# Kernel optimization log

Measured on AMD Instinct MI355X. Metric: run time of the kernel, lower is better.

Reference implementation:

```python
import jax, jax.numpy as jnp
import numpy as np

B, T, V, H, L = 32, 128, 50257, 1024, 2


def setup_inputs() -> dict:
    key = jax.random.key(0)
    ks = jax.random.split(key, 8)
    s_in = 0.02   # small init to keep gates unsaturated
    return {
        "tokens": jax.random.randint(ks[0], (B, T), 0, V, dtype=jnp.int32),
        "embedding": jax.random.normal(ks[1], (V, H), jnp.float32) * s_in,
        "W_ih": jax.random.normal(ks[2], (L, 4 * H, H), jnp.float32) * s_in,
        "W_hh": jax.random.normal(ks[3], (L, 4 * H, H), jnp.float32) * s_in,
        "b_ih": jax.random.normal(ks[4], (L, 4 * H), jnp.float32) * s_in,
        "b_hh": jax.random.normal(ks[5], (L, 4 * H), jnp.float32) * s_in,
        "W_out": jax.random.normal(ks[6], (V, H), jnp.float32) * s_in,
        "b_out": jax.random.normal(ks[7], (V,), jnp.float32) * s_in,
        "h0": jnp.zeros((L, B, H), jnp.float32),
        "c0": jnp.zeros((L, B, H), jnp.float32),
    }


def reference(tokens, embedding, W_ih, W_hh, b_ih, b_hh, W_out, b_out, h0, c0):
    # Teacher-forced LSTM LM: embed -> L-layer LSTM (PyTorch gate order i,f,g,o)
    # -> vocab projection -> log-softmax. Dropout is identity (p=0 / eval).
    x = embedding[tokens]                      # [B,T,H]
    xs = jnp.swapaxes(x, 0, 1)                 # [T,B,H] time-major for scan
    n_layers = W_ih.shape[0]

    def step(carry, x_t):
        h, c = carry                           # each [L,B,H]
        inp = x_t
        hs, cs = [], []
        for l in range(n_layers):
            gates = inp @ W_ih[l].T + b_ih[l] + h[l] @ W_hh[l].T + b_hh[l]  # [B,4H]
            i_g, f_g, g_g, o_g = jnp.split(gates, 4, axis=-1)
            i_g = jax.nn.sigmoid(i_g)
            f_g = jax.nn.sigmoid(f_g)
            g_g = jnp.tanh(g_g)
            o_g = jax.nn.sigmoid(o_g)
            c_new = f_g * c[l] + i_g * g_g
            h_new = o_g * jnp.tanh(c_new)
            hs.append(h_new)
            cs.append(c_new)
            inp = h_new
        return (jnp.stack(hs), jnp.stack(cs)), inp

    (hT, cT), outs = jax.lax.scan(step, (h0, c0), xs)   # outs: [T,B,H]
    outs = jnp.swapaxes(outs, 0, 1)                     # [B,T,H]
    logits = outs @ W_out.T + b_out                     # [B,T,V]
    logp = jax.nn.log_softmax(logits, axis=-1)
    return logp, hT, cT
```

## Files before the change

### kernel.cpp

```cpp
#include <hip/hip_runtime.h>
#include <cstdint>
#include <cstddef>

#define DEVI __device__ __forceinline__

typedef __attribute__((ext_vector_type(8))) short short8;
typedef __attribute__((ext_vector_type(4))) float f32x4;
using u16 = unsigned short;

constexpr int BSZ = 32, TSZ = 128, VSZ = 50257, HSZ = 1024;
constexpr int M4 = BSZ * TSZ;
constexpr int FH = 4 * HSZ;
constexpr long long OUT_LOGP = (long long)M4 * VSZ;
constexpr int NWRK = 192;
constexpr int LDSB = 147584;
constexpr int LDBF = 50258;

DEVI u16 f2bf(float f) {
  unsigned u = __float_as_uint(f);
  unsigned r = (u + 0x7fffu + ((u >> 16) & 1u)) >> 16;
  return (u16)r;
}
DEVI float bf2f(u16 u) { return __uint_as_float(((unsigned)u) << 16); }
DEVI float sigm(float x) { return 1.f / (1.f + __expf(-x)); }
DEVI float tanh_fast(float x) { return 1.f - 2.f / (1.f + __expf(2.f * x)); }

DEVI f32x4 mfma16(short8 a, short8 b, f32x4 c) {
  return __builtin_amdgcn_mfma_f32_16x16x32_bf16(a, b, c, 0, 0, 0);
}

DEVI void gld16(const void* g, void* l) {
  auto gp = (const __attribute__((address_space(1))) unsigned int*)g;
  auto lp = (__attribute__((address_space(3))) unsigned int*)l;
  __builtin_amdgcn_global_load_lds(gp, lp, 16, 0, 0);
}

DEVI void cohld16x16(const u16* base, short8 (&d)[16]) {
  asm volatile(
      "global_load_dwordx4 %0, %16, off sc0 sc1\n\t"
      "global_load_dwordx4 %1, %16, off offset:64 sc0 sc1\n\t"
      "global_load_dwordx4 %2, %16, off offset:128 sc0 sc1\n\t"
      "global_load_dwordx4 %3, %16, off offset:192 sc0 sc1\n\t"
      "global_load_dwordx4 %4, %16, off offset:256 sc0 sc1\n\t"
      "global_load_dwordx4 %5, %16, off offset:320 sc0 sc1\n\t"
      "global_load_dwordx4 %6, %16, off offset:384 sc0 sc1\n\t"
      "global_load_dwordx4 %7, %16, off offset:448 sc0 sc1\n\t"
      "global_load_dwordx4 %8, %16, off offset:512 sc0 sc1\n\t"
      "global_load_dwordx4 %9, %16, off offset:576 sc0 sc1\n\t"
      "global_load_dwordx4 %10, %16, off offset:640 sc0 sc1\n\t"
      "global_load_dwordx4 %11, %16, off offset:704 sc0 sc1\n\t"
      "global_load_dwordx4 %12, %16, off offset:768 sc0 sc1\n\t"
      "global_load_dwordx4 %13, %16, off offset:832 sc0 sc1\n\t"
      "global_load_dwordx4 %14, %16, off offset:896 sc0 sc1\n\t"
      "global_load_dwordx4 %15, %16, off offset:960 sc0 sc1\n\t"
      "s_waitcnt vmcnt(0)"
      : "=&v"(d[0]), "=&v"(d[1]), "=&v"(d[2]), "=&v"(d[3]),
        "=&v"(d[4]), "=&v"(d[5]), "=&v"(d[6]), "=&v"(d[7]),
        "=&v"(d[8]), "=&v"(d[9]), "=&v"(d[10]), "=&v"(d[11]),
        "=&v"(d[12]), "=&v"(d[13]), "=&v"(d[14]), "=&v"(d[15])
      : "v"(base)
      : "memory");
}
DEVI void cohst2_u16(u16* p0, u16 v0, u16* p1, u16 v1) {
  asm volatile(
      "global_store_short %0, %2, off sc0 sc1\n\t"
      "global_store_short %1, %3, off sc0 sc1\n\t"
      "s_waitcnt vmcnt(0)"
      :: "v"(p0), "v"(p1), "v"((unsigned)v0), "v"((unsigned)v1)
      : "memory");
}
DEVI void cohst1_u16(u16* p0, u16 v0) {
  asm volatile(
      "global_store_short %0, %1, off sc0 sc1\n\t"
      "s_waitcnt vmcnt(0)"
      :: "v"(p0), "v"((unsigned)v0)
      : "memory");
}
DEVI void flagst(unsigned* p, unsigned v) {
  __hip_atomic_store(p, v, __ATOMIC_RELAXED, __HIP_MEMORY_SCOPE_AGENT);
}
DEVI unsigned flagld(const unsigned* p) {
  return __hip_atomic_load(p, __ATOMIC_RELAXED, __HIP_MEMORY_SCOPE_AGENT);
}

DEVI void wait64(const unsigned* f, unsigned g, int l) {
  while (!__all((int)(flagld(f + l) >= g))) __builtin_amdgcn_s_sleep(1);
}
DEVI void wait128(const unsigned* f, unsigned g, int l) {
  for (;;) {
    unsigned a = flagld(f + l);
    unsigned b = flagld(f + 64 + l);
    if (__all((int)((a >= g) && (b >= g)))) break;
    __builtin_amdgcn_s_sleep(1);
  }
}

__global__ void prep_misc(const float* __restrict__ bih, const float* __restrict__ bhh,
                          float* __restrict__ bias0, float* __restrict__ rowsum,
                          unsigned* __restrict__ bar) {
  int i = blockIdx.x * 256 + threadIdx.x;
  if (i < FH) { bias0[i] = bih[i] + bhh[i]; rowsum[i] = 0.f; }
  if (i < 1024) bar[i] = 0u;
}

__global__ void prep_h(const float* __restrict__ h0, u16* __restrict__ H0,
                       u16* __restrict__ h1init) {
  int i = blockIdx.x * 256 + threadIdx.x;
  H0[i] = f2bf(h0[i]);
  h1init[i] = f2bf(h0[BSZ * HSZ + i]);
}

__global__ void cvt_bf16(const float* __restrict__ src, u16* __restrict__ dst, int n4) {
  int i = blockIdx.x * blockDim.x + threadIdx.x;
  int stride = gridDim.x * blockDim.x;
  for (; i < n4; i += stride) {
    float4 v = ((const float4*)src)[i];
    ushort4 o; o.x = f2bf(v.x); o.y = f2bf(v.y); o.z = f2bf(v.z); o.w = f2bf(v.w);
    ((ushort4*)dst)[i] = o;
  }
}

__global__ __launch_bounds__(256) void embed_kernel(const int* __restrict__ tok,
                                                    const float* __restrict__ emb,
                                                    u16* __restrict__ X) {
  int m = blockIdx.x;
  int t = m >> 5, b = m & 31;
  int token = tok[b * TSZ + t];
  const float4* src = (const float4*)(emb + (size_t)token * HSZ);
  int i = threadIdx.x;
  float4 v = src[i];
  ushort4 o; o.x = f2bf(v.x); o.y = f2bf(v.y); o.z = f2bf(v.z); o.w = f2bf(v.w);
  *(ushort4*)(X + (size_t)m * HSZ + i * 4) = o;
}

template <int EPI, bool BCVT, int MAP>
__global__ __launch_bounds__(256) void gemm_bt(const u16* __restrict__ A,
                                               const void* __restrict__ Bsrc,
                                               void* __restrict__ Cout,
                                               const float* __restrict__ bias,
                                               float* __restrict__ rowsum,
                                               int nm, int nn, int N, int K, int ldc) {
  __shared__ char smemg[16384];
  u16* As = (u16*)smemg;
  u16* Bs = (u16*)(smemg + 8192);
  float* epi = (float*)smemg;
  const int tid = threadIdx.x;
  int gsz = nm * nn;
  int id = blockIdx.x;
  int bm, bn;
  if constexpr (MAP == 1) {
    const int xcd = id & 7, idx = id >> 3;
    bn = idx >> 2;
    bm = (xcd << 2) + (idx & 3);
  } else {
    int wg = ((gsz & 7) == 0) ? (id % 8) * (gsz >> 3) + (id >> 3) : id;
    bm = wg % nm; bn = wg / nm;
  }
  const int m0 = bm * 128, n0 = bn * 128;
  const int l = tid & 63, wid = tid >> 6;
  const int wm = wid >> 1, wn = wid & 1;

  const int srow = tid >> 2, sq = tid & 3;
  const int arow0 = m0 + srow, arow1 = m0 + 64 + srow;
  int brow0 = n0 + srow;      if (brow0 > N - 1) brow0 = N - 1;
  int brow1 = n0 + 64 + srow; if (brow1 > N - 1) brow1 = N - 1;

  const u16* Bbf = (const u16*)Bsrc;
  const float* Bf32 = (const float*)Bsrc;
  u16* AsW = As + (size_t)(tid >> 6) * 512;
  u16* BsW = Bs + (size_t)(tid >> 6) * 512;

  f32x4 acc[4][4];
  f32x4 z = {0.f, 0.f, 0.f, 0.f};
#pragma unroll
  for (int a = 0; a < 4; ++a)
#pragma unroll
    for (int b = 0; b < 4; ++b) acc[a][b] = z;

  for (int k0 = 0; k0 < K; k0 += 32) {
    gld16(A + (size_t)arow0 * K + k0 + sq * 8, AsW);
    gld16(A + (size_t)arow1 * K + k0 + sq * 8, AsW + 2048);
    if (!BCVT) {
      gld16(Bbf + (size_t)brow0 * K + k0 + sq * 8, BsW);
      gld16(Bbf + (size_t)brow1 * K + k0 + sq * 8, BsW + 2048);
    } else {
      const float* s0 = Bf32 + (size_t)brow0 * K + k0 + sq * 8;
      const float* s1 = Bf32 + (size_t)brow1 * K + k0 + sq * 8;
      float4 x0 = *(const float4*)s0, y0 = *(const float4*)(s0 + 4);
      float4 x1 = *(const float4*)s1, y1 = *(const float4*)(s1 + 4);
      short8 v0, v1;
      v0[0]=(short)f2bf(x0.x); v0[1]=(short)f2bf(x0.y); v0[2]=(short)f2bf(x0.z); v0[3]=(short)f2bf(x0.w);
      v0[4]=(short)f2bf(y0.x); v0[5]=(short)f2bf(y0.y); v0[6]=(short)f2bf(y0.z); v0[7]=(short)f2bf(y0.w);
      v1[0]=(short)f2bf(x1.x); v1[1]=(short)f2bf(x1.y); v1[2]=(short)f2bf(x1.z); v1[3]=(short)f2bf(x1.w);
      v1[4]=(short)f2bf(y1.x); v1[5]=(short)f2bf(y1.y); v1[6]=(short)f2bf(y1.z); v1[7]=(short)f2bf(y1.w);
      *(short8*)&Bs[(size_t)tid * 8] = v0;
      *(short8*)&Bs[(size_t)tid * 8 + 2048] = v1;
    }
    __syncthreads();
    short8 af[4], bfr[4];
#pragma unroll
    for (int x = 0; x < 4; ++x) {
      int ar = wm * 64 + x * 16 + (l & 15);
      af[x] = *(const short8*)&As[ar * 32 + ((l >> 4) << 3)];
      int br = wn * 64 + x * 16 + (l & 15);
      bfr[x] = *(const short8*)&Bs[br * 32 + ((l >> 4) << 3)];
    }
#pragma unroll
    for (int mf = 0; mf < 4; ++mf)
#pragma unroll
      for (int nf = 0; nf < 4; ++nf)
        acc[mf][nf] = mfma16(af[mf], bfr[nf], acc[mf][nf]);
    __syncthreads();
  }

  if constexpr (EPI == 2) {
    u16* C = (u16*)Cout;
#pragma unroll
    for (int mf = 0; mf < 4; ++mf) {
      int rbase = m0 + wm * 64 + mf * 16 + ((l >> 4) << 2);
      float bvr[4];
#pragma unroll
      for (int j = 0; j < 4; ++j) bvr[j] = bias[rbase + j];
#pragma unroll
      for (int nf = 0; nf < 4; ++nf) {
        int cg = n0 + wn * 64 + nf * 16 + (l & 15);
#pragma unroll
        for (int j = 0; j < 4; ++j)
          C[(size_t)(rbase + j) * ldc + cg] = f2bf(acc[mf][nf][j] + bvr[j]);
      }
    }
  } else if constexpr (EPI == 3) {
    u16* C = (u16*)Cout;
    float* ep = epi + wid * 1024;
    const int lq4 = l >> 4, l15e = l & 15;
    float bv[4];
#pragma unroll
    for (int nf = 0; nf < 4; ++nf) {
      int cg = n0 + wn * 64 + nf * 16 + l15e;
      bv[nf] = (cg < N) ? bias[cg] : 0.f;
    }
    const int r8 = l >> 3, c8 = l & 7;
    const int colb8 = n0 + wn * 64 + c8 * 8;
#pragma unroll
    for (int mf = 0; mf < 4; ++mf) {
#pragma unroll
      for (int nf = 0; nf < 4; ++nf)
#pragma unroll
        for (int j = 0; j < 4; ++j)
          ep[(lq4 * 4 + j) * 64 + nf * 16 + l15e] = acc[mf][nf][j] + bv[nf];
      asm volatile("s_waitcnt lgkmcnt(0)" ::: "memory");
      __builtin_amdgcn_sched_barrier(0);
#pragma unroll
      for (int pass = 0; pass < 2; ++pass) {
        const int rr = pass * 8 + r8;
        f32x4 v0 = *(const f32x4*)&ep[rr * 64 + c8 * 8];
        f32x4 v1 = *(const f32x4*)&ep[rr * 64 + c8 * 8 + 4];
        const int row = m0 + wm * 64 + mf * 16 + rr;
        float e = 0.f;
        if (colb8 + 7 < N) {
          short8 o;
          o[0]=(short)f2bf(v0[0]); o[1]=(short)f2bf(v0[1]);
          o[2]=(short)f2bf(v0[2]); o[3]=(short)f2bf(v0[3]);
          o[4]=(short)f2bf(v1[0]); o[5]=(short)f2bf(v1[1]);
          o[6]=(short)f2bf(v1[2]); o[7]=(short)f2bf(v1[3]);
          *(short8*)&C[(size_t)row * ldc + colb8] = o;
          e = __expf(v0[0]) + __expf(v0[1]) + __expf(v0[2]) + __expf(v0[3]) +
              __expf(v1[0]) + __expf(v1[1]) + __expf(v1[2]) + __expf(v1[3]);
        } else {
#pragma unroll
          for (int kk = 0; kk < 8; ++kk) {
            float fv = (kk < 4) ? v0[kk] : v1[kk - 4];
            if (colb8 + kk < N) {
              C[(size_t)row * ldc + colb8 + kk] = f2bf(fv);
              e += __expf(fv);
            }
          }
        }
        e += __shfl_xor(e, 1, 8); e += __shfl_xor(e, 2, 8); e += __shfl_xor(e, 4, 8);
        if (c8 == 0) atomicAdd(&rowsum[row], e);
      }
      asm volatile("s_waitcnt lgkmcnt(0)" ::: "memory");
      __builtin_amdgcn_sched_barrier(0);
    }
  } else {
    float* C = (float*)Cout;
    float* ep = epi + wid * 1024;
    const int lq4 = l >> 4, l15e = l & 15;
    float bv[4];
#pragma unroll
    for (int nf = 0; nf < 4; ++nf) {
      int cg = n0 + wn * 64 + nf * 16 + l15e;
      bv[nf] = (cg < N) ? bias[cg] : 0.f;
    }
    const int colbase = n0 + wn * 64 + l15e * 4;
#pragma unroll
    for (int mf = 0; mf < 4; ++mf) {
#pragma unroll
      for (int nf = 0; nf < 4; ++nf)
#pragma unroll
        for (int j = 0; j < 4; ++j)
          ep[(lq4 * 4 + j) * 64 + nf * 16 + l15e] = acc[mf][nf][j] + bv[nf];
      asm volatile("s_waitcnt lgkmcnt(0)" ::: "memory");
      __builtin_amdgcn_sched_barrier(0);
#pragma unroll
      for (int pass = 0; pass < 4; ++pass) {
        const int rr = pass * 4 + lq4;
        f32x4 v = *(const f32x4*)&ep[rr * 64 + l15e * 4];
        const int row = m0 + wm * 64 + mf * 16 + rr;
        float e = 0.f;
        if (colbase + 3 < N) {
          *(f32x4*)&C[(size_t)row * ldc + colbase] = v;
          e = __expf(v[0]) + __expf(v[1]) + __expf(v[2]) + __expf(v[3]);
        } else {
#pragma unroll
          for (int kk = 0; kk < 4; ++kk)
            if (colbase + kk < N) {
              C[(size_t)row * ldc + colbase + kk] = v[kk];
              e += __expf(v[kk]);
            }
        }
        e += __shfl_xor(e, 1, 16); e += __shfl_xor(e, 2, 16);
        e += __shfl_xor(e, 4, 16); e += __shfl_xor(e, 8, 16);
        if (l15e == 0) atomicAdd(&rowsum[row], e);
      }
      asm volatile("s_waitcnt lgkmcnt(0)" ::: "memory");
      __builtin_amdgcn_sched_barrier(0);
    }
  }
}

struct LstmArgs {
  const u16* G0T;
  const float* Wih;
  const float* Whh;
  const float* bih, *bhh, *c0;
  u16* H0;
  u16* H1;
  const u16* h1init;
  float* out_hc;
  unsigned* bar;
};

DEVI void stage_row_q(const float* src, char* row, int sw, int q) {
  for (int kk = 0; kk < 256; kk += 8) {
    float4 x = *(const float4*)(src + kk);
    float4 y = *(const float4*)(src + kk + 4);
    short8 v;
    v[0]=(short)f2bf(x.x); v[1]=(short)f2bf(x.y); v[2]=(short)f2bf(x.z); v[3]=(short)f2bf(x.w);
    v[4]=(short)f2bf(y.x); v[5]=(short)f2bf(y.y); v[6]=(short)f2bf(y.z); v[7]=(short)f2bf(y.w);
    const int kbyte = (q * 256 + kk) * 2;
    *(short8*)(row + (kbyte ^ sw)) = v;
  }
}

DEVI short8 ldsB(const char* lds, int r, int kbyte) {
  return *(const short8*)(lds + (size_t)r * 2048 + (kbyte ^ ((r & 7) << 4)));
}

DEVI void part_wr(float* part, int wstride_log2, int wv, int R, int lq, f32x4 v) {
  *(f32x4*)&part[(wv << wstride_log2) + (R << 4) + ((lq ^ (R & 3)) << 2)] = v;
}
DEVI float part_rd(const float* part, int wstride_log2, int wv, int R, int c) {
  return part[(wv << wstride_log2) + (R << 4) + ((((c >> 2) ^ (R & 3)) << 2)) + (c & 3)];
}

__global__ __launch_bounds__(256, 1) void lstm_coop(LstmArgs A) {
  extern __shared__ char smem[];
  const int wg = blockIdx.x, tid = threadIdx.x;
  const int wv = tid >> 6, l = tid & 63;
  const int l15 = l & 15, lq = l >> 4;
  const int bh = wv >> 1, kh = wv & 1;

  if (wg < 64) {
    char* WL = smem;
    float* part = (float*)(smem + 131072);
    const int j0 = wg << 4;
    {
      const int R = tid >> 2, q = tid & 3;
      const int grow = ((R >> 4) << 10) + j0 + (R & 15);
      stage_row_q(A.Whh + (size_t)grow * HSZ + q * 256, WL + (size_t)R * 2048,
                  (R & 7) << 4, q);
    }
    const int uu = tid & 15, bb = tid >> 4;
    float cst[2];
    cst[0] = A.c0[(size_t)bb * HSZ + j0 + uu];
    cst[1] = A.c0[(size_t)(bb + 16) * HSZ + j0 + uu];
    __syncthreads();
    unsigned* myflag = A.bar + wg;

    for (int t = 0; t < TSZ; ++t) {
      float g0v[4][2];
      {
        const int col = t * 32;
#pragma unroll
        for (int g4 = 0; g4 < 4; ++g4) {
          const u16* gp = A.G0T + (size_t)((g4 << 10) + j0 + uu) * M4 + col;
          g0v[g4][0] = bf2f(gp[bb]);
          g0v[g4][1] = bf2f(gp[bb + 16]);
        }
      }
      if (t > 0) wait64(A.bar, (unsigned)t, l);
      const u16* hprev = A.H0 + (size_t)t * (BSZ * HSZ);
      const u16* hb = hprev + (size_t)(bh * 16 + l15) * HSZ + (kh << 9) + (lq << 3);
      short8 a[16];
      cohld16x16(hb, a);
      __builtin_amdgcn_sched_barrier(0);
      f32x4 acc[4];
      { f32x4 z = {0.f,0.f,0.f,0.f}; acc[0]=z; acc[1]=z; acc[2]=z; acc[3]=z; }
#pragma unroll
      for (int k = 0; k < 16; ++k) {
        const int kbyte = (((kh << 4) + k) << 6) + (lq << 4);
#pragma unroll
        for (int tr = 0; tr < 4; ++tr)
          acc[tr] = mfma16(a[k], ldsB(WL, (tr << 4) + l15, kbyte), acc[tr]);
      }
#pragma unroll
      for (int tr = 0; tr < 4; ++tr)
        part_wr(part, 10, wv, (tr << 4) + l15, lq, acc[tr]);
      __syncthreads();
      const bool last = (t == TSZ - 1);
      u16* hnext = A.H0 + (size_t)(t + 1) * (BSZ * HSZ);
      u16 hv[2];
#pragma unroll
      for (int pp = 0; pp < 2; ++pp) {
        const int b = bb + (pp << 4);
        float gi = g0v[0][pp], gf = g0v[1][pp], gg = g0v[2][pp], go = g0v[3][pp];
#pragma unroll
        for (int kh2 = 0; kh2 < 2; ++kh2) {
          const int w2 = (pp << 1) | kh2;
          gi += part_rd(part, 10, w2, uu, bb);
          gf += part_rd(part, 10, w2, 16 + uu, bb);
          gg += part_rd(part, 10, w2, 32 + uu, bb);
          go += part_rd(part, 10, w2, 48 + uu, bb);
        }
        float i_ = sigm(gi), f_ = sigm(gf), g_ = tanh_fast(gg), o_ = sigm(go);
        float c_ = f_ * cst[pp] + i_ * g_;
        cst[pp] = c_;
        float h_ = o_ * tanh_fast(c_);
        hv[pp] = f2bf(h_);
        if (last) {
          A.out_hc[(size_t)b * HSZ + j0 + uu] = h_;
          A.out_hc[2 * BSZ * HSZ + (size_t)b * HSZ + j0 + uu] = c_;
        }
      }
      cohst2_u16(hnext + (size_t)bb * HSZ + j0 + uu, hv[0],
                 hnext + (size_t)(bb + 16) * HSZ + j0 + uu, hv[1]);
      __syncthreads();
      if (tid == 0) flagst(myflag, (unsigned)(t + 1));
    }
  } else {
    char* WxL = smem;
    char* WhL = smem + 65536;
    float* part = (float*)(smem + 131072);
    float* biasL = (float*)(smem + 139264);
    const int lw = wg - 64;
    const int j1 = lw << 3;
    {
      const int rr = tid >> 2, q = tid & 3;
      const int r = rr & 31;
      const int grow = FH + ((r >> 3) << 10) + j1 + (r & 7);
      const float* base = (rr >= 32) ? A.Whh : A.Wih;
      char* dst = ((rr >= 32) ? WhL : WxL) + (size_t)r * 2048;
      stage_row_q(base + (size_t)grow * HSZ + q * 256, dst, (r & 7) << 4, q);
    }
    if (tid < 32) {
      const int grow = FH + ((tid >> 3) << 10) + j1 + (tid & 7);
      biasL[tid] = A.bih[grow] + A.bhh[grow];
    }
    const int uu = tid & 7, b1 = tid >> 3;
    float cst = A.c0[BSZ * HSZ + (size_t)b1 * HSZ + j1 + uu];
    __syncthreads();
    unsigned* myflag = A.bar + 64 + lw;

    for (int t = 0; t < TSZ; ++t) {
      wait64(A.bar, (unsigned)(t + 1), l);
      const u16* x1 = A.H0 + (size_t)(t + 1) * (BSZ * HSZ);
      const u16* xb = x1 + (size_t)(bh * 16 + l15) * HSZ + (kh << 9) + (lq << 3);
      short8 ax[16];
      cohld16x16(xb, ax);
      __builtin_amdgcn_sched_barrier(0);
      f32x4 acc[2];
      { f32x4 z = {0.f,0.f,0.f,0.f}; acc[0]=z; acc[1]=z; }
#pragma unroll
      for (int k = 0; k < 16; ++k) {
        const int kbyte = (((kh << 4) + k) << 6) + (lq << 4);
        acc[0] = mfma16(ax[k], ldsB(WxL, l15, kbyte), acc[0]);
        acc[1] = mfma16(ax[k], ldsB(WxL, 16 + l15, kbyte), acc[1]);
      }
      if (t > 0) wait128(A.bar + 64, (unsigned)t, l);
      const u16* hp = (t == 0) ? A.h1init : A.H1 + (size_t)(t - 1) * HSZ;
      const size_t hstr = (t == 0) ? (size_t)HSZ : (size_t)TSZ * HSZ;
      const u16* hbp = hp + (size_t)(bh * 16 + l15) * hstr + (kh << 9) + (lq << 3);
      short8 ah[16];
      cohld16x16(hbp, ah);
      __builtin_amdgcn_sched_barrier(0);
#pragma unroll
      for (int k = 0; k < 16; ++k) {
        const int kbyte = (((kh << 4) + k) << 6) + (lq << 4);
        acc[0] = mfma16(ah[k], ldsB(WhL, l15, kbyte), acc[0]);
        acc[1] = mfma16(ah[k], ldsB(WhL, 16 + l15, kbyte), acc[1]);
      }
#pragma unroll
      for (int tr = 0; tr < 2; ++tr)
        part_wr(part, 9, wv, (tr << 4) + l15, lq, acc[tr]);
      __syncthreads();
      const bool last = (t == TSZ - 1);
      {
        const int c = b1 & 15, ph = b1 >> 4;
        float gi = biasL[uu], gf = biasL[8 + uu], gg = biasL[16 + uu], go = biasL[24 + uu];
#pragma unroll
        for (int kh2 = 0; kh2 < 2; ++kh2) {
          const int w2 = (ph << 1) | kh2;
          gi += part_rd(part, 9, w2, uu, c);
          gf += part_rd(part, 9, w2, 8 + uu, c);
          gg += part_rd(part, 9, w2, 16 + uu, c);
          go += part_rd(part, 9, w2, 24 + uu, c);
        }
        float i_ = sigm(gi), f_ = sigm(gf), g_ = tanh_fast(gg), o_ = sigm(go);
        float c_ = f_ * cst + i_ * g_;
        cst = c_;
        float h_ = o_ * tanh_fast(c_);
        cohst1_u16(A.H1 + (size_t)b1 * (TSZ * HSZ) + (size_t)t * HSZ + j1 + uu, f2bf(h_));
        if (last) {
          A.out_hc[BSZ * HSZ + (size_t)b1 * HSZ + j1 + uu] = h_;
          A.out_hc[3 * BSZ * HSZ + (size_t)b1 * HSZ + j1 + uu] = c_;
        }
      }
      __syncthreads();
      if (tid == 0) flagst(myflag, (unsigned)(t + 1));
    }
  }
}

__global__ void lse_kernel(float* __restrict__ rowsum, int n) {
  int i = blockIdx.x * 256 + threadIdx.x;
  if (i < n) rowsum[i] = logf(rowsum[i]);
}

__global__ __launch_bounds__(256) void lsm_finish(float* __restrict__ C,
                                                  const float* __restrict__ lse, int Vd) {
  int row = blockIdx.y;
  size_t start = (size_t)row * (size_t)Vd;
  float s = lse[row];
  int i = blockIdx.x * 256 + threadIdx.x;
  int col = i * 4;
  if (col + 3 < Vd) {
    f32x4* p = (f32x4*)(C + start + col);
    f32x4 v = *p;
    v[0] -= s; v[1] -= s; v[2] -= s; v[3] -= s;
    *p = v;
  } else {
    for (int j = col; j < Vd; ++j) C[start + j] -= s;
  }
}

__global__ __launch_bounds__(256) void lsm_finish_bf(const u16* __restrict__ L,
                                                     float* __restrict__ out,
                                                     const float* __restrict__ lse,
                                                     int Vd, int ldl) {
  int row = blockIdx.y;
  float s = lse[row];
  int col = blockIdx.x * 2048 + threadIdx.x * 8;
  const u16* lp = L + (size_t)row * ldl;
  float* op = out + (size_t)row * Vd;
  if (col + 7 < Vd) {
    short8 v = *(const short8*)(lp + col);
    f32x4 a, b;
    a[0] = bf2f((u16)v[0]) - s; a[1] = bf2f((u16)v[1]) - s;
    a[2] = bf2f((u16)v[2]) - s; a[3] = bf2f((u16)v[3]) - s;
    b[0] = bf2f((u16)v[4]) - s; b[1] = bf2f((u16)v[5]) - s;
    b[2] = bf2f((u16)v[6]) - s; b[3] = bf2f((u16)v[7]) - s;
    *(f32x4*)(op + col) = a;
    *(f32x4*)(op + col + 4) = b;
  } else {
    for (int j = col; j < Vd; ++j) op[j] = bf2f(lp[j]) - s;
  }
}

extern "C" void kernel_launch(void* const* d_in, const int* in_sizes, int n_in,
                              void* d_out, int out_size, void* d_ws, size_t ws_size,
                              hipStream_t stream) {
  const int* tokens = (const int*)d_in[0];
  const float* emb = (const float*)d_in[1];
  const float* Wih = (const float*)d_in[2];
  const float* Whh = (const float*)d_in[3];
  const float* bih = (const float*)d_in[4];
  const float* bhh = (const float*)d_in[5];
  const float* Wout = (const float*)d_in[6];
  const float* bout = (const float*)d_in[7];
  const float* h0 = (const float*)d_in[8];
  const float* c0 = (const float*)d_in[9];
  float* out = (float*)d_out;

  char* w = (char*)d_ws;
  size_t o = 0;
  u16* Xbf = (u16*)(w + o);    o += (size_t)M4 * HSZ * 2;
  u16* Wih0bf = (u16*)(w + o); o += (size_t)FH * HSZ * 2;
  u16* G0T = (u16*)(w + o);    o += (size_t)FH * M4 * 2;
  u16* H0 = (u16*)(w + o);     o += (size_t)(TSZ + 1) * BSZ * HSZ * 2;
  u16* H1 = (u16*)(w + o);     o += (size_t)BSZ * TSZ * HSZ * 2;
  u16* h1init = (u16*)(w + o); o += (size_t)BSZ * HSZ * 2;
  float* bias0 = (float*)(w + o);  o += FH * 4;
  float* rowsum = (float*)(w + o); o += M4 * 4;
  unsigned* bar = (unsigned*)(w + o); o += 4096;
  u16* Woutbf = (u16*)(w + o);
  size_t need_full = o + (size_t)VSZ * HSZ * 2;
  u16* Lbf = (u16*)(w + need_full);
  size_t need_lbf = need_full + (size_t)M4 * LDBF * 2;
  const bool bcvt = (ws_size < need_full);
  const bool bf16c = (ws_size >= need_lbf);

  prep_misc<<<16, 256, 0, stream>>>(bih, bhh, bias0, rowsum, bar);
  prep_h<<<128, 256, 0, stream>>>(h0, H0, h1init);
  cvt_bf16<<<2048, 256, 0, stream>>>(Wih, Wih0bf, FH * HSZ / 4);
  if (!bcvt)
    cvt_bf16<<<4096, 256, 0, stream>>>(Wout, Woutbf, (int)((size_t)VSZ * HSZ / 4));
  embed_kernel<<<M4, 256, 0, stream>>>(tokens, emb, Xbf);
  gemm_bt<2, false, 0><<<32 * 32, 256, 0, stream>>>(Wih0bf, Xbf, G0T, bias0, nullptr,
                                                    32, 32, M4, HSZ, M4);

  LstmArgs la{G0T, Wih, Whh, bih, bhh, c0, H0, H1, h1init,
              out + (size_t)OUT_LOGP, bar};
  void* kargs[] = {&la};
  hipFuncSetAttribute((const void*)lstm_coop, hipFuncAttributeMaxDynamicSharedMemorySize, LDSB);
  hipLaunchCooperativeKernel((const void*)lstm_coop, dim3(NWRK), dim3(256), kargs, LDSB, stream);

  const int nn = (VSZ + 127) / 128;
  if (bf16c) {
    gemm_bt<3, false, 1><<<32 * nn, 256, 0, stream>>>(H1, Woutbf, Lbf, bout, rowsum,
                                                      32, nn, VSZ, HSZ, LDBF);
  } else if (!bcvt) {
    gemm_bt<1, false, 1><<<32 * nn, 256, 0, stream>>>(H1, Woutbf, out, bout, rowsum,
                                                      32, nn, VSZ, HSZ, VSZ);
  } else {
    gemm_bt<1, true, 1><<<32 * nn, 256, 0, stream>>>(H1, Wout, out, bout, rowsum,
                                                     32, nn, VSZ, HSZ, VSZ);
  }

  lse_kernel<<<16, 256, 0, stream>>>(rowsum, M4);
  if (bf16c)
    lsm_finish_bf<<<dim3(25, M4), 256, 0, stream>>>(Lbf, out, rowsum, VSZ, LDBF);
  else
    lsm_finish<<<dim3((VSZ + 1023) / 1024, M4), 256, 0, stream>>>(out, rowsum, VSZ);
}
```

Baseline: 1.807 ms.

## Overlap Wout bf16 conversion with LSTM recurrence using spare cooperative blocks

```diff
diff --git a/kernel.cpp b/kernel.cpp
--- a/kernel.cpp
+++ b/kernel.cpp
@@ -13,6 +13,7 @@
 constexpr int FH = 4 * HSZ;
 constexpr long long OUT_LOGP = (long long)M4 * VSZ;
 constexpr int NWRK = 192;
+constexpr int NBLK = 256;
 constexpr int LDSB = 147584;
 constexpr int LDBF = 50258;
 
@@ -339,6 +340,9 @@
   const u16* h1init;
   float* out_hc;
   unsigned* bar;
+  const float* Wout;
+  u16* Woutbf;
+  int docvt;
 };
 
 DEVI void stage_row_q(const float* src, char* row, int sw, int q) {
@@ -448,7 +452,7 @@
       __syncthreads();
       if (tid == 0) flagst(myflag, (unsigned)(t + 1));
     }
-  } else {
+  } else if (wg < NWRK) {
     char* WxL = smem;
     char* WhL = smem + 65536;
     float* part = (float*)(smem + 131072);
@@ -529,6 +533,19 @@
       __syncthreads();
       if (tid == 0) flagst(myflag, (unsigned)(t + 1));
     }
+  } else {
+    if (A.docvt) {
+      const int n4 = (int)((size_t)VSZ * HSZ / 4);
+      int i = (wg - NWRK) * 256 + tid;
+      const int stride = 64 * 256;
+      const float4* src = (const float4*)A.Wout;
+      ushort4* dst = (ushort4*)A.Woutbf;
+      for (; i < n4; i += stride) {
+        float4 v = src[i];
+        ushort4 o; o.x = f2bf(v.x); o.y = f2bf(v.y); o.z = f2bf(v.z); o.w = f2bf(v.w);
+        dst[i] = o;
+      }
+    }
   }
 }
 
@@ -556,10 +573,10 @@
 
 __global__ __launch_bounds__(256) void lsm_finish_bf(const u16* __restrict__ L,
                                                      float* __restrict__ out,
-                                                     const float* __restrict__ lse,
+                                                     const float* __restrict__ rowsum,
                                                      int Vd, int ldl) {
   int row = blockIdx.y;
-  float s = lse[row];
+  float s = logf(rowsum[row]);
   int col = blockIdx.x * 2048 + threadIdx.x * 8;
   const u16* lp = L + (size_t)row * ldl;
   float* op = out + (size_t)row * Vd;
@@ -613,33 +630,30 @@
   prep_misc<<<16, 256, 0, stream>>>(bih, bhh, bias0, rowsum, bar);
   prep_h<<<128, 256, 0, stream>>>(h0, H0, h1init);
   cvt_bf16<<<2048, 256, 0, stream>>>(Wih, Wih0bf, FH * HSZ / 4);
-  if (!bcvt)
-    cvt_bf16<<<4096, 256, 0, stream>>>(Wout, Woutbf, (int)((size_t)VSZ * HSZ / 4));
   embed_kernel<<<M4, 256, 0, stream>>>(tokens, emb, Xbf);
   gemm_bt<2, false, 0><<<32 * 32, 256, 0, stream>>>(Wih0bf, Xbf, G0T, bias0, nullptr,
                                                     32, 32, M4, HSZ, M4);
 
   LstmArgs la{G0T, Wih, Whh, bih, bhh, c0, H0, H1, h1init,
-              out + (size_t)OUT_LOGP, bar};
+              out + (size_t)OUT_LOGP, bar, Wout, Woutbf, bcvt ? 0 : 1};
   void* kargs[] = {&la};
   hipFuncSetAttribute((const void*)lstm_coop, hipFuncAttributeMaxDynamicSharedMemorySize, LDSB);
-  hipLaunchCooperativeKernel((const void*)lstm_coop, dim3(NWRK), dim3(256), kargs, LDSB, stream);
+  hipLaunchCooperativeKernel((const void*)lstm_coop, dim3(NBLK), dim3(256), kargs, LDSB, stream);
 
   const int nn = (VSZ + 127) / 128;
   if (bf16c) {
     gemm_bt<3, false, 1><<<32 * nn, 256, 0, stream>>>(H1, Woutbf, Lbf, bout, rowsum,
                                                       32, nn, VSZ, HSZ, LDBF);
+    lsm_finish_bf<<<dim3(25, M4), 256, 0, stream>>>(Lbf, out, rowsum, VSZ, LDBF);
   } else if (!bcvt) {
     gemm_bt<1, false, 1><<<32 * nn, 256, 0, stream>>>(H1, Woutbf, out, bout, rowsum,
                                                       32, nn, VSZ, HSZ, VSZ);
+    lse_kernel<<<16, 256, 0, stream>>>(rowsum, M4);
+    lsm_finish<<<dim3((VSZ + 1023) / 1024, M4), 256, 0, stream>>>(out, rowsum, VSZ);
   } else {
     gemm_bt<1, true, 1><<<32 * nn, 256, 0, stream>>>(H1, Wout, out, bout, rowsum,
                                                      32, nn, VSZ, HSZ, VSZ);
-  }
-
-  lse_kernel<<<16, 256, 0, stream>>>(rowsum, M4);
-  if (bf16c)
-    lsm_finish_bf<<<dim3(25, M4), 256, 0, stream>>>(Lbf, out, rowsum, VSZ, LDBF);
-  else
+    lse_kernel<<<16, 256, 0, stream>>>(rowsum, M4);
     lsm_finish<<<dim3((VSZ + 1023) / 1024, M4), 256, 0, stream>>>(out, rowsum, VSZ);
-}
+  }
+}
```

Measured after the change: 1.749 ms. -3.2%, faster.
